# Performance work log

Measured on AMD Instinct MI355X. Metric: run time of the kernel, lower is better.

## Reference

```python
import jax, jax.numpy as jnp
import numpy as np

R, C, B, E, H = 128, 256, 1, 768, 12
DK = E // H


def setup_inputs() -> dict:
    key = jax.random.key(0)
    ks = jax.random.split(key, 6)
    x = jax.random.normal(ks[0], (R, C, B, E), dtype=jnp.float32)
    padding_mask = jnp.zeros((B, R, C), dtype=bool)  # all positions valid
    w_scale = 0.02
    Wq = jax.random.normal(ks[1], (E, E), dtype=jnp.float32) * w_scale
    Wk = jax.random.normal(ks[2], (E, E), dtype=jnp.float32) * w_scale
    Wv = jax.random.normal(ks[3], (E, E), dtype=jnp.float32) * w_scale
    Wo = jax.random.normal(ks[4], (E, E), dtype=jnp.float32) * w_scale
    bq = jnp.zeros((E,), jnp.float32)
    bk = jnp.zeros((E,), jnp.float32)
    bv = jnp.zeros((E,), jnp.float32)
    bo = jnp.zeros((E,), jnp.float32)
    return {"x": x, "padding_mask": padding_mask, "Wq": Wq, "bq": bq,
            "Wk": Wk, "bk": bk, "Wv": Wv, "bv": bv, "Wo": Wo, "bo": bo}


def reference(x, padding_mask, Wq, bq, Wk, bk, Wv, bv, Wo, bo):
    # x: (n_rows=i, n_cols=c, batch=n, embed)
    n_rows, n_cols, batch, embed = x.shape
    d_k = embed // H
    scaling = d_k ** -0.5
    # torch Linear: y = x @ W.T + b
    q = (x @ Wq.T + bq).reshape(n_rows, n_cols, batch, H, d_k) * scaling
    k = (x @ Wk.T + bk).reshape(n_rows, n_cols, batch, H, d_k)
    v = (x @ Wv.T + bv).reshape(n_rows, n_cols, batch, H, d_k)
    # attention over the row axis, independent per column and batch
    attn = jnp.einsum('icnhd,jcnhd->hcnij', q, k)  # (H, C, B, R, R)
    # padding_mask (n, i, c) -> (1, c, n, 1, j), masked keys get -10000
    m = jnp.transpose(padding_mask, (2, 0, 1))[None, :, :, None, :]
    attn = jnp.where(m, jnp.float32(-10000.0), attn)
    probs = jax.nn.softmax(attn, axis=-1)
    # dropout is identity in eval/reference mode
    ctx = jnp.einsum('hcnij,jcnhd->icnhd', probs, v)
    ctx = ctx.reshape(n_rows, n_cols, batch, embed)
    out = ctx @ Wo.T + bo
    return out, probs
```

## Files before the change

kernel.cpp:

```cpp
#include <hip/hip_runtime.h>
#include <hip/hip_bf16.h>

typedef __attribute__((ext_vector_type(8))) short bf16x8;
typedef __attribute__((ext_vector_type(4))) float f32x4;
typedef __attribute__((ext_vector_type(8))) unsigned short u16x8;

#define RR 128
#define CC 256
#define EE 768
#define HH 12
#define DKK 64
#define NQKV 2304

__device__ __forceinline__ unsigned short f2bf(float f) {
  union { float f; unsigned u; } v; v.f = f;
  unsigned u = v.u;
  unsigned r = (u + 0x7fffu + ((u >> 16) & 1u)) >> 16;
  return (unsigned short)r;
}

__device__ __forceinline__ void gload16(const unsigned short* g, char* l) {
  __builtin_amdgcn_global_load_lds((const __attribute__((address_space(1))) void*)g,
                                   (__attribute__((address_space(3))) void*)l, 16, 0, 0);
}

__global__ void cast_f32_to_bf16(const float* __restrict__ src,
                                 unsigned short* __restrict__ dst, int n8) {
  int t = blockIdx.x * 256 + threadIdx.x;
  if (t >= n8) return;
  const float4* s = (const float4*)src + (size_t)t * 2;
  float4 a = s[0], b = s[1];
  u16x8 o;
  o[0] = f2bf(a.x); o[1] = f2bf(a.y); o[2] = f2bf(a.z); o[3] = f2bf(a.w);
  o[4] = f2bf(b.x); o[5] = f2bf(b.y); o[6] = f2bf(b.z); o[7] = f2bf(b.w);
  *(u16x8*)(dst + (size_t)t * 8) = o;
}


#define SBAR() do { __builtin_amdgcn_sched_barrier(0); __builtin_amdgcn_s_barrier(); } while (0)
#define SBAR2() do { __builtin_amdgcn_sched_barrier(0); __builtin_amdgcn_s_barrier(); __builtin_amdgcn_sched_barrier(0); } while (0)
#define WAITL() do { asm volatile("s_waitcnt lgkmcnt(0)" ::: "memory"); __builtin_amdgcn_sched_barrier(0); } while (0)
#define WAITV(N) asm volatile("s_waitcnt vmcnt(" #N ")" ::: "memory")

template <int OUTMODE>
__global__ __launch_bounds__(512, 2) void gemm256(
    const unsigned short* __restrict__ A, const unsigned short* __restrict__ Bw,
    void* __restrict__ OutP, const float* __restrict__ bias0,
    const float* __restrict__ bias1, const float* __restrict__ bias2) {
  __shared__ __align__(16) char smem[131072];
  const int nwg = gridDim.x;
  const int chunk = nwg >> 3;
  const int swz = ((int)blockIdx.x & 7) * chunk + ((int)blockIdx.x >> 3);
  const int bm = swz % 128, bn = swz / 128;
  const int r0 = bm << 8, c0 = bn << 8;

  const int tid = threadIdx.x;
  const int w = tid >> 6, lane = tid & 63;
  const int wr = w >> 2, wc = w & 3;
  const int lr = lane & 15, lg = lane >> 4;
  const int l8 = lane >> 3, l7 = lane & 7;
  const int swzc = (l7 ^ (l8 & 7)) << 3;
  const unsigned short* pa = A + (size_t)(r0 + l8) * EE + swzc;
  const unsigned short* pb = Bw + (size_t)(c0 + l8) * EE + swzc;
  const int j0 = w, j1 = w + 8;

  const int aoff = (wr << 14) + (lr << 7);
  const int boff = 32768 + ((wc >> 1) << 14) + ((wc & 1) << 13) + (lr << 7);
  const int sw0 = ((0 + lg) ^ (lr & 7)) << 4;
  const int sw1 = ((4 + lg) ^ (lr & 7)) << 4;

  f32x4 acc[8][4] = {};
  bf16x8 aA[4], aB[4], aC[4], aD[4], bA[4], bB[4];

#define STAGE(s, H, t)                                                        \
  do {                                                                        \
    const unsigned short* _src = ((H) < 2 ? pa : pb) +                        \
        (size_t)(((H) & 1) * 128) * EE + (size_t)(t) * 64;                    \
    char* _d = smem + (s) * 65536 + ((H) >= 2 ? 32768 : 0) + ((H) & 1) * 16384; \
    gload16(_src + (size_t)j0 * 8 * EE, _d + j0 * 1024);                      \
    gload16(_src + (size_t)j1 * 8 * EE, _d + j1 * 1024);                      \
  } while (0)

#define RD_A(dst, g, SW, s)                                                   \
  _Pragma("unroll") for (int _m = 0; _m < 4; ++_m)                            \
      dst[_m] = *(const bf16x8*)(smem + (s) * 65536 + aoff + (g) * 8192 +     \
                                 _m * 2048 + (SW));

#define RD_B(dst, SW, s)                                                      \
  _Pragma("unroll") for (int _n = 0; _n < 4; ++_n)                            \
      dst[_n] = *(const bf16x8*)(smem + (s) * 65536 + boff + _n * 2048 + (SW));

#define MM(g, ar, br)                                                         \
  do {                                                                        \
    __builtin_amdgcn_s_setprio(1);                                            \
    _Pragma("unroll") for (int _i = 0; _i < 4; ++_i)                          \
        _Pragma("unroll") for (int _j = 0; _j < 4; ++_j)                      \
            acc[(g) * 4 + _i][_j] = __builtin_amdgcn_mfma_f32_16x16x32_bf16(  \
                ar[_i], br[_j], acc[(g) * 4 + _i][_j], 0, 0, 0);              \
    __builtin_amdgcn_s_setprio(0);                                            \
  } while (0)

#define ITER(ii, LASTF)                                                        \
  do {                                                                         \
    const int t0 = 2 * (ii), t1 = t0 + 1;                                      \
     RD_A(aA, 0, sw0, 0); RD_B(bA, sw0, 0); STAGE(1, 1, t1);             \
    SBAR(); WAITL(); MM(0, aA, bA); SBAR2();                                   \
     RD_A(aB, 1, sw0, 0); RD_A(aC, 0, sw1, 0); STAGE(1, 2, t1);          \
    SBAR(); WAITL(); MM(1, aB, bA); SBAR2();                                   \
     RD_B(bB, sw1, 0); RD_A(aD, 1, sw1, 0); STAGE(1, 3, t1);             \
    SBAR(); WAITL(); MM(0, aC, bB); SBAR2();                                   \
     if (!(LASTF)) { STAGE(0, 0, t0 + 2); WAITV(2); } else { WAITV(0); } \
    SBAR(); WAITL(); MM(1, aD, bB); SBAR2();                                   \
     RD_A(aA, 0, sw0, 1); RD_B(bA, sw0, 1);                              \
    if (!(LASTF)) STAGE(0, 1, t0 + 2);                                         \
    SBAR(); WAITL(); MM(0, aA, bA); SBAR2();                                   \
     RD_A(aB, 1, sw0, 1); RD_A(aC, 0, sw1, 1);                           \
    if (!(LASTF)) STAGE(0, 2, t0 + 2);                                         \
    SBAR(); WAITL(); MM(1, aB, bA); SBAR2();                                   \
     RD_B(bB, sw1, 1); RD_A(aD, 1, sw1, 1);                              \
    if (!(LASTF)) STAGE(0, 3, t0 + 2);                                         \
    SBAR(); WAITL(); MM(0, aC, bB); SBAR2();                                   \
     if (!(LASTF)) { STAGE(1, 0, t1 + 2); WAITV(2); }                    \
    SBAR(); WAITL(); MM(1, aD, bB); SBAR2();                                   \
  } while (0)

  STAGE(0, 0, 0); STAGE(0, 1, 0); STAGE(0, 2, 0); STAGE(0, 3, 0);
  STAGE(1, 0, 1);
  WAITV(2);
  SBAR2();

#pragma unroll 1
  for (int it = 0; it < 5; ++it) { ITER(it, 0); }
  ITER(5, 1);

#undef STAGE
#undef RD_A
#undef RD_B
#undef MM
#undef ITER

  if constexpr (OUTMODE == 1) {
    unsigned short* sm = (unsigned short*)smem;
    const int mat = bn / 3;
    const float scale = (mat == 0) ? 0.125f : 1.0f;
    const float* bp = (mat == 0) ? bias0 : (mat == 1 ? bias1 : bias2);
    const int cb = c0 - mat * 768;
    float bv4[4];
#pragma unroll
    for (int n = 0; n < 4; ++n) bv4[n] = bp[cb + (wc << 6) + (n << 4) + lr];
#pragma unroll
    for (int m = 0; m < 8; ++m)
#pragma unroll
      for (int n = 0; n < 4; ++n)
#pragma unroll
        for (int r = 0; r < 4; ++r) {
          int row = (wr << 7) + (m << 4) + (lg << 2) + r;
          int col = (wc << 6) + (n << 4) + lr;
          sm[row * 256 + col] = f2bf((acc[m][n][r] + bv4[n]) * scale);
        }
    __syncthreads();
    unsigned short* out = (unsigned short*)OutP;
#pragma unroll
    for (int p = 0; p < 16; ++p) {
      int idx = p * 512 + tid;
      int row = idx >> 5, c16 = idx & 31;
      *(u16x8*)(out + (size_t)(r0 + row) * NQKV + c0 + c16 * 8) =
          *(const u16x8*)(sm + idx * 8);
    }
  } else {
    float* out = (float*)OutP;
    float bv4[4];
#pragma unroll
    for (int n = 0; n < 4; ++n) bv4[n] = bias0[c0 + (wc << 6) + (n << 4) + lr];
#pragma unroll
    for (int m = 0; m < 8; ++m)
#pragma unroll
      for (int n = 0; n < 4; ++n)
#pragma unroll
        for (int r = 0; r < 4; ++r) {
          int row = (wr << 7) + (m << 4) + (lg << 2) + r;
          int col = (wc << 6) + (n << 4) + lr;
          out[(size_t)(r0 + row) * EE + c0 + col] = acc[m][n][r] + bv4[n];
        }
  }
}

__global__ __launch_bounds__(256, 2) void attn_kernel(
    const unsigned short* __restrict__ qkv, const unsigned char* __restrict__ pmask,
    float* __restrict__ probs, unsigned short* __restrict__ ctx) {
  __shared__ unsigned short ks[128 * 72];
  __shared__ unsigned short vt[64 * 136];
  __shared__ unsigned short ps[128 * 136];
  const int bx = blockIdx.x;
  const int c = bx / HH, h = bx - (bx / HH) * HH;
  const int tid = threadIdx.x;
  const int wid = tid >> 6, lane = tid & 63;
  const int lr = lane & 15, lg = lane >> 4;
  const int wr = wid;
  const size_t hoff = (size_t)h * DKK;

#pragma unroll
  for (int p = 0; p < 4; ++p) {
    int chunk = p * 256 + tid;
    int j = chunk >> 3, d0 = (chunk & 7) << 3;
    const unsigned short* base = qkv + ((size_t)j * CC + c) * NQKV + hoff;
    bf16x8 kv = *(const bf16x8*)(base + 768 + d0);
    *(bf16x8*)&ks[j * 72 + d0] = kv;
    bf16x8 vv = *(const bf16x8*)(base + 1536 + d0);
#pragma unroll
    for (int u = 0; u < 8; ++u) vt[(d0 + u) * 136 + j] = (unsigned short)vv[u];
  }

  bf16x8 qf[2][2];
#pragma unroll
  for (int m = 0; m < 2; ++m)
#pragma unroll
    for (int kk = 0; kk < 2; ++kk) {
      int qi = (wr << 5) + (m << 4) + lr;
      qf[m][kk] = *(const bf16x8*)(qkv + ((size_t)qi * CC + c) * NQKV + hoff +
                                   kk * 32 + (lg << 3));
    }

  __syncthreads();

  f32x4 s[2][8] = {};
#pragma unroll
  for (int kk = 0; kk < 2; ++kk) {
    bf16x8 kf[8];
#pragma unroll
    for (int n = 0; n < 8; ++n)
      kf[n] = *(const bf16x8*)&ks[(n * 16 + lr) * 72 + kk * 32 + (lg << 3)];
#pragma unroll
    for (int m = 0; m < 2; ++m)
#pragma unroll
      for (int n = 0; n < 8; ++n)
        s[m][n] = __builtin_amdgcn_mfma_f32_16x16x32_bf16(qf[m][kk], kf[n],
                                                          s[m][n], 0, 0, 0);
  }

#pragma unroll
  for (int n = 0; n < 8; ++n) {
    if (pmask[(size_t)(n * 16 + lr) * CC + c] != 0) {
      f32x4 neg = {-10000.0f, -10000.0f, -10000.0f, -10000.0f};
      s[0][n] = neg;
      s[1][n] = neg;
    }
  }

  float inv_[2][4];
#pragma unroll
  for (int m = 0; m < 2; ++m) {
    f32x4 mx = s[m][0];
#pragma unroll
    for (int n = 1; n < 8; ++n)
#pragma unroll
      for (int r = 0; r < 4; ++r) mx[r] = fmaxf(mx[r], s[m][n][r]);
#pragma unroll
    for (int r = 0; r < 4; ++r) {
      float t = mx[r];
      t = fmaxf(t, __shfl_xor(t, 1));
      t = fmaxf(t, __shfl_xor(t, 2));
      t = fmaxf(t, __shfl_xor(t, 4));
      t = fmaxf(t, __shfl_xor(t, 8));
      mx[r] = t;
    }
    f32x4 sum = {};
#pragma unroll
    for (int n = 0; n < 8; ++n)
#pragma unroll
      for (int r = 0; r < 4; ++r) {
        float e = exp2f((s[m][n][r] - mx[r]) * 1.44269504f);
        s[m][n][r] = e;
        sum[r] += e;
      }
#pragma unroll
    for (int r = 0; r < 4; ++r) {
      float t = sum[r];
      t += __shfl_xor(t, 1);
      t += __shfl_xor(t, 2);
      t += __shfl_xor(t, 4);
      t += __shfl_xor(t, 8);
      inv_[m][r] = __builtin_amdgcn_rcpf(t);
    }
  }

  const size_t pbase = ((size_t)h * CC + c) * (size_t)(128 * 128);
#pragma unroll
  for (int m = 0; m < 2; ++m)
#pragma unroll
    for (int n = 0; n < 8; ++n)
#pragma unroll
      for (int r = 0; r < 4; ++r) {
        float pv = s[m][n][r] * inv_[m][r];
        int i = (wr << 5) + (m << 4) + (lg << 2) + r;
        int j = (n << 4) + lr;
        probs[pbase + (size_t)i * 128 + j] = pv;
        ps[i * 136 + j] = f2bf(pv);
      }

  __syncthreads();

  f32x4 o[2][4] = {};
#pragma unroll
  for (int kk = 0; kk < 4; ++kk) {
    bf16x8 pa[2], vb[4];
#pragma unroll
    for (int m = 0; m < 2; ++m)
      pa[m] = *(const bf16x8*)&ps[((wr << 5) + (m << 4) + lr) * 136 + kk * 32 + (lg << 3)];
#pragma unroll
    for (int n = 0; n < 4; ++n)
      vb[n] = *(const bf16x8*)&vt[((n << 4) + lr) * 136 + kk * 32 + (lg << 3)];
#pragma unroll
    for (int m = 0; m < 2; ++m)
#pragma unroll
      for (int n = 0; n < 4; ++n)
        o[m][n] = __builtin_amdgcn_mfma_f32_16x16x32_bf16(pa[m], vb[n], o[m][n], 0, 0, 0);
  }

#pragma unroll
  for (int m = 0; m < 2; ++m)
#pragma unroll
    for (int n = 0; n < 4; ++n)
#pragma unroll
      for (int r = 0; r < 4; ++r) {
        int i = (wr << 5) + (m << 4) + (lg << 2) + r;
        int d = (n << 4) + lr;
        ctx[((size_t)i * CC + c) * EE + hoff + d] = f2bf(o[m][n][r]);
      }
}

extern "C" void kernel_launch(void* const* d_in, const int* in_sizes, int n_in,
                              void* d_out, int out_size, void* d_ws, size_t ws_size,
                              hipStream_t stream) {
  const float* x = (const float*)d_in[0];
  const unsigned char* pm = (const unsigned char*)d_in[1];
  const float* Wq = (const float*)d_in[2];
  const float* bq = (const float*)d_in[3];
  const float* Wk = (const float*)d_in[4];
  const float* bk = (const float*)d_in[5];
  const float* Wv = (const float*)d_in[6];
  const float* bv = (const float*)d_in[7];
  const float* Wo = (const float*)d_in[8];
  const float* bo = (const float*)d_in[9];

  unsigned short* ws = (unsigned short*)d_ws;
  unsigned short* xb = ws;
  unsigned short* qkv = xb + 25165824;
  unsigned short* wqkv = qkv + 75497472;
  unsigned short* wo = wqkv + 1769472;

  float* outp = (float*)d_out;
  float* probs = outp + 25165824;

  cast_f32_to_bf16<<<12288, 256, 0, stream>>>(x, xb, 3145728);
  cast_f32_to_bf16<<<288, 256, 0, stream>>>(Wq, wqkv, 73728);
  cast_f32_to_bf16<<<288, 256, 0, stream>>>(Wk, wqkv + 589824, 73728);
  cast_f32_to_bf16<<<288, 256, 0, stream>>>(Wv, wqkv + 1179648, 73728);
  cast_f32_to_bf16<<<288, 256, 0, stream>>>(Wo, wo, 73728);

  gemm256<1><<<1152, 512, 0, stream>>>(xb, wqkv, (void*)qkv, bq, bk, bv);
  attn_kernel<<<CC * HH, 256, 0, stream>>>(qkv, pm, probs, xb );
  gemm256<0><<<384, 512, 0, stream>>>(xb, wo, (void*)outp, bo, nullptr, nullptr);
}
```

Before: 347.3 us.

## Write Q/K/V in per-column-head contiguous layout and coalesce ctx stores

The QKV projection epilogue now writes Q, K and V into separate buffers laid out as [column][head][row][d], so each attention block reads one contiguous 16KB tile instead of strided rows. Attention stages its ctx output through shared memory and writes it column-major with 16-byte vector stores. The output GEMM remaps rows to restore the original (row, column) order. The five cast launches are merged into one kernel. This trades scattered epilogue stores in the GEMMs for coalesced loads in attention.

After: 328.9 us. 5.3% less time.

```diff
diff --git a/kernel.cpp b/kernel.cpp
--- a/kernel.cpp
+++ b/kernel.cpp
@@ -24,15 +24,28 @@
                                    (__attribute__((address_space(3))) void*)l, 16, 0, 0);
 }
 
-__global__ void cast_f32_to_bf16(const float* __restrict__ src,
-                                 unsigned short* __restrict__ dst, int n8) {
-  int t = blockIdx.x * 256 + threadIdx.x;
-  if (t >= n8) return;
+__global__ void cast_all(const float* __restrict__ x, const float* __restrict__ w0,
+                         const float* __restrict__ w1, const float* __restrict__ w2,
+                         const float* __restrict__ w3, unsigned short* __restrict__ xb,
+                         unsigned short* __restrict__ wdst) {
+  int b = blockIdx.x;
+  const float* src;
+  unsigned short* dst;
+  int t;
+  if (b < 12288) {
+    src = x; dst = xb; t = b * 256 + (int)threadIdx.x;
+  } else {
+    int bb = b - 12288;
+    int m = bb / 288;
+    src = (m == 0) ? w0 : (m == 1) ? w1 : (m == 2) ? w2 : w3;
+    dst = wdst + (size_t)m * 589824;
+    t = (bb - m * 288) * 256 + (int)threadIdx.x;
+  }
   const float4* s = (const float4*)src + (size_t)t * 2;
-  float4 a = s[0], b = s[1];
+  float4 a = s[0], bq = s[1];
   u16x8 o;
   o[0] = f2bf(a.x); o[1] = f2bf(a.y); o[2] = f2bf(a.z); o[3] = f2bf(a.w);
-  o[4] = f2bf(b.x); o[5] = f2bf(b.y); o[6] = f2bf(b.z); o[7] = f2bf(b.w);
+  o[4] = f2bf(bq.x); o[5] = f2bf(bq.y); o[6] = f2bf(bq.z); o[7] = f2bf(bq.w);
   *(u16x8*)(dst + (size_t)t * 8) = o;
 }
 
@@ -159,13 +172,17 @@
           sm[row * 256 + col] = f2bf((acc[m][n][r] + bv4[n]) * scale);
         }
     __syncthreads();
-    unsigned short* out = (unsigned short*)OutP;
+    unsigned short* outm = (unsigned short*)OutP + (size_t)mat * 25165824;
+    const int hbase = cb >> 6;
+    const int i_idx = r0 >> 8;
 #pragma unroll
     for (int p = 0; p < 16; ++p) {
       int idx = p * 512 + tid;
-      int row = idx >> 5, c16 = idx & 31;
-      *(u16x8*)(out + (size_t)(r0 + row) * NQKV + c0 + c16 * 8) =
-          *(const u16x8*)(sm + idx * 8);
+      int row = idx >> 5;
+      int hl = (idx >> 3) & 3;
+      int d8 = idx & 7;
+      *(u16x8*)(outm + ((((size_t)(row * HH + hbase + hl)) << 7 | i_idx) << 6) + d8 * 8) =
+          *(const u16x8*)(sm + row * 256 + hl * 64 + d8 * 8);
     }
   } else {
     float* out = (float*)OutP;
@@ -178,15 +195,17 @@
       for (int n = 0; n < 4; ++n)
 #pragma unroll
         for (int r = 0; r < 4; ++r) {
-          int row = (wr << 7) + (m << 4) + (lg << 2) + r;
+          int u = r0 + (wr << 7) + (m << 4) + (lg << 2) + r;
+          int t = ((u & 127) << 8) | (u >> 7);
           int col = (wc << 6) + (n << 4) + lr;
-          out[(size_t)(r0 + row) * EE + c0 + col] = acc[m][n][r] + bv4[n];
+          out[(size_t)t * EE + c0 + col] = acc[m][n][r] + bv4[n];
         }
   }
 }
 
 __global__ __launch_bounds__(256, 2) void attn_kernel(
-    const unsigned short* __restrict__ qkv, const unsigned char* __restrict__ pmask,
+    const unsigned short* __restrict__ qatt, const unsigned short* __restrict__ katt,
+    const unsigned short* __restrict__ vatt, const unsigned char* __restrict__ pmask,
     float* __restrict__ probs, unsigned short* __restrict__ ctx) {
   __shared__ unsigned short ks[128 * 72];
   __shared__ unsigned short vt[64 * 136];
@@ -197,16 +216,18 @@
   const int wid = tid >> 6, lane = tid & 63;
   const int lr = lane & 15, lg = lane >> 4;
   const int wr = wid;
-  const size_t hoff = (size_t)h * DKK;
+  const size_t blk = ((size_t)(c * HH + h)) << 13;
+  const unsigned short* qb = qatt + blk;
+  const unsigned short* kb = katt + blk;
+  const unsigned short* vb = vatt + blk;
 
 #pragma unroll
   for (int p = 0; p < 4; ++p) {
     int chunk = p * 256 + tid;
     int j = chunk >> 3, d0 = (chunk & 7) << 3;
-    const unsigned short* base = qkv + ((size_t)j * CC + c) * NQKV + hoff;
-    bf16x8 kv = *(const bf16x8*)(base + 768 + d0);
+    bf16x8 kv = *(const bf16x8*)(kb + j * 64 + d0);
     *(bf16x8*)&ks[j * 72 + d0] = kv;
-    bf16x8 vv = *(const bf16x8*)(base + 1536 + d0);
+    bf16x8 vv = *(const bf16x8*)(vb + j * 64 + d0);
 #pragma unroll
     for (int u = 0; u < 8; ++u) vt[(d0 + u) * 136 + j] = (unsigned short)vv[u];
   }
@@ -217,8 +238,7 @@
 #pragma unroll
     for (int kk = 0; kk < 2; ++kk) {
       int qi = (wr << 5) + (m << 4) + lr;
-      qf[m][kk] = *(const bf16x8*)(qkv + ((size_t)qi * CC + c) * NQKV + hoff +
-                                   kk * 32 + (lg << 3));
+      qf[m][kk] = *(const bf16x8*)(qb + qi * 64 + kk * 32 + (lg << 3));
     }
 
   __syncthreads();
@@ -303,20 +323,21 @@
   f32x4 o[2][4] = {};
 #pragma unroll
   for (int kk = 0; kk < 4; ++kk) {
-    bf16x8 pa[2], vb[4];
+    bf16x8 pa[2], vbr[4];
 #pragma unroll
     for (int m = 0; m < 2; ++m)
       pa[m] = *(const bf16x8*)&ps[((wr << 5) + (m << 4) + lr) * 136 + kk * 32 + (lg << 3)];
 #pragma unroll
     for (int n = 0; n < 4; ++n)
-      vb[n] = *(const bf16x8*)&vt[((n << 4) + lr) * 136 + kk * 32 + (lg << 3)];
+      vbr[n] = *(const bf16x8*)&vt[((n << 4) + lr) * 136 + kk * 32 + (lg << 3)];
 #pragma unroll
     for (int m = 0; m < 2; ++m)
 #pragma unroll
       for (int n = 0; n < 4; ++n)
-        o[m][n] = __builtin_amdgcn_mfma_f32_16x16x32_bf16(pa[m], vb[n], o[m][n], 0, 0, 0);
-  }
-
+        o[m][n] = __builtin_amdgcn_mfma_f32_16x16x32_bf16(pa[m], vbr[n], o[m][n], 0, 0, 0);
+  }
+
+  unsigned short* cbuf = ks;
 #pragma unroll
   for (int m = 0; m < 2; ++m)
 #pragma unroll
@@ -325,8 +346,16 @@
       for (int r = 0; r < 4; ++r) {
         int i = (wr << 5) + (m << 4) + (lg << 2) + r;
         int d = (n << 4) + lr;
-        ctx[((size_t)i * CC + c) * EE + hoff + d] = f2bf(o[m][n][r]);
+        cbuf[i * 64 + d] = f2bf(o[m][n][r]);
       }
+  __syncthreads();
+#pragma unroll
+  for (int p = 0; p < 4; ++p) {
+    int chunk = p * 256 + tid;
+    int i = chunk >> 3, d8 = chunk & 7;
+    *(u16x8*)(ctx + ((size_t)c * 128 + i) * EE + h * 64 + d8 * 8) =
+        *(const u16x8*)(cbuf + i * 64 + d8 * 8);
+  }
 }
 
 extern "C" void kernel_launch(void* const* d_in, const int* in_sizes, int n_in,
@@ -346,19 +375,15 @@
   unsigned short* ws = (unsigned short*)d_ws;
   unsigned short* xb = ws;
   unsigned short* qkv = xb + 25165824;
-  unsigned short* wqkv = qkv + 75497472;
-  unsigned short* wo = wqkv + 1769472;
+  unsigned short* wcast = qkv + 75497472;
 
   float* outp = (float*)d_out;
   float* probs = outp + 25165824;
 
-  cast_f32_to_bf16<<<12288, 256, 0, stream>>>(x, xb, 3145728);
-  cast_f32_to_bf16<<<288, 256, 0, stream>>>(Wq, wqkv, 73728);
-  cast_f32_to_bf16<<<288, 256, 0, stream>>>(Wk, wqkv + 589824, 73728);
-  cast_f32_to_bf16<<<288, 256, 0, stream>>>(Wv, wqkv + 1179648, 73728);
-  cast_f32_to_bf16<<<288, 256, 0, stream>>>(Wo, wo, 73728);
-
-  gemm256<1><<<1152, 512, 0, stream>>>(xb, wqkv, (void*)qkv, bq, bk, bv);
-  attn_kernel<<<CC * HH, 256, 0, stream>>>(qkv, pm, probs, xb );
-  gemm256<0><<<384, 512, 0, stream>>>(xb, wo, (void*)outp, bo, nullptr, nullptr);
-}
+  cast_all<<<13440, 256, 0, stream>>>(x, Wq, Wk, Wv, Wo, xb, wcast);
+  gemm256<1><<<1152, 512, 0, stream>>>(xb, wcast, (void*)qkv, bq, bk, bv);
+  attn_kernel<<<CC * HH, 256, 0, stream>>>(qkv, qkv + 25165824, qkv + 50331648,
+                                           pm, probs, xb );
+  gemm256<0><<<384, 512, 0, stream>>>(xb, wcast + 1769472, (void*)outp, bo,
+                                      nullptr, nullptr);
+}
```
